# Kernel tuning notes

Measured on AMD Instinct MI355X. Metric: run time of the kernel, lower is better.

Reference implementation:

```python
import jax, jax.numpy as jnp
import numpy as np

GROUP_SIZE = 128


def setup_inputs() -> dict:
    key = jax.random.key(0)
    k1, k2, k3, k4 = jax.random.split(key, 4)
    B, S, IN, OUT = 4, 2048, 4096, 11008
    n_groups = IN // GROUP_SIZE
    x = jax.random.normal(k1, (B, S, IN), dtype=jnp.float32)
    # packed int4: two nibbles per byte -> [OUT, IN//2]
    weight_quantized = jax.random.randint(k2, (OUT, IN // 2), 0, 256, dtype=jnp.int32)
    # per-(row,group) scale > 0 and zero point (stored fp16 in torch, math done in fp32)
    weight_scale = jax.random.uniform(k3, (OUT, n_groups), dtype=jnp.float32, minval=0.001, maxval=0.05)
    weight_zero_point = jax.random.normal(k4, (OUT, n_groups), dtype=jnp.float32) * 0.1
    return {"x": x, "weight_quantized": weight_quantized,
            "weight_scale": weight_scale, "weight_zero_point": weight_zero_point}


def reference(x, weight_quantized, weight_scale, weight_zero_point):
    out_f = weight_quantized.shape[0]
    n_groups = weight_scale.shape[1]
    # unpack nibbles: high first, then low (matches torch.stack([high, low], -1))
    high = (weight_quantized >> 4) & 0xF
    low = weight_quantized & 0xF
    unpacked = jnp.stack([high, low], axis=-1).reshape(out_f, -1).astype(jnp.float32)  # [OUT, IN]
    # grouped dequant: w = q * scale_g + zp_g
    w = unpacked.reshape(out_f, n_groups, GROUP_SIZE)
    w = w * weight_scale[:, :, None] + weight_zero_point[:, :, None]
    w = w.reshape(out_f, -1)  # [OUT, IN]
    # F.linear: x @ w.T
    return jnp.einsum('bsi,oi->bso', x, w)
```

## Files before the change

### kernel.cpp

```cpp
#include <hip/hip_runtime.h>
#include <cstdint>
#include <cstddef>

#define M_TOT 8192
#define N_TOT 11008
#define K_TOT 4096
#define WROW_PACK 2048
#define NG 32

#define BM 256
#define BN 256
#define BKT 32
#define NSLOT 4
#define NT (K_TOT / BKT)
#define NBM2 (M_TOT / BM)
#define NBN2 (N_TOT / BN)
#define NWG2 (NBM2 * NBN2)
#define SLOT_USH 16384
#define LDS_BYTES (NSLOT * SLOT_USH * 2)

typedef __attribute__((ext_vector_type(8))) short short8;
typedef __attribute__((ext_vector_type(4))) float f32x4;
typedef unsigned short ushort_t;

__device__ __forceinline__ unsigned int pack2_bf16(float lo, float hi) {
    return __builtin_amdgcn_perm(__float_as_uint(hi), __float_as_uint(lo), 0x07060302u);
}

__device__ __forceinline__ unsigned int dequant_pair(int q, float s, float z) {
    float wh = (float)(q >> 4) * s + z;
    float wl = (float)(q & 15) * s + z;
    return pack2_bf16(wh, wl);
}

__device__ __forceinline__ void gload_lds16(const void* g, void* l) {
    __builtin_amdgcn_global_load_lds(
        (const __attribute__((address_space(1))) unsigned int*)g,
        (__attribute__((address_space(3))) unsigned int*)l,
        16, 0, 0);
}

__global__ __launch_bounds__(256)
void convert_x_kernel(const float4* __restrict__ xin, uint4* __restrict__ xout) {
    const size_t t = (size_t)blockIdx.x * 256 + threadIdx.x;
    const float4 v0 = xin[2 * t];
    const float4 v1 = xin[2 * t + 1];
    xout[t] = make_uint4(pack2_bf16(v0.x, v0.y), pack2_bf16(v0.z, v0.w),
                         pack2_bf16(v1.x, v1.y), pack2_bf16(v1.z, v1.w));
}

__global__ __launch_bounds__(256)
void dequant_w_kernel(const int4* __restrict__ wq4,
                      const float* __restrict__ wsc,
                      const float* __restrict__ wzp,
                      uint4* __restrict__ wout) {
    const size_t t = (size_t)blockIdx.x * 256 + threadIdx.x;
    const int row = (int)(t >> 9);
    const int c4  = (int)(t & 511);
    const int g   = c4 >> 4;
    const float s = wsc[(size_t)row * NG + g];
    const float z = wzp[(size_t)row * NG + g];
    const int4 q = wq4[t];
    wout[t] = make_uint4(dequant_pair(q.x, s, z), dequant_pair(q.y, s, z),
                         dequant_pair(q.z, s, z), dequant_pair(q.w, s, z));
}

__global__ __launch_bounds__(512, 2)
void gemm_bf16_256(const ushort_t* __restrict__ A,
                   const ushort_t* __restrict__ B,
                   float* __restrict__ out)
{
    extern __shared__ ushort_t lds[];

    const int tid  = threadIdx.x;
    const int lane = tid & 63;
    const int wv   = tid >> 6;
    const int wm   = wv >> 2;
    const int wn   = wv & 3;
    const int l15  = lane & 15;
    const int quad = lane >> 4;

    const int bid = blockIdx.x;
    const int swz = (bid & 7) * (NWG2 >> 3) + (bid >> 3);
    const int bm  = swz / NBN2;
    const int bn  = swz % NBN2;
    const size_t m0 = (size_t)bm * BM;
    const size_t n0 = (size_t)bn * BN;

    const int srow = tid >> 2;
    const int lc   = (tid & 3) ^ (srow & 3);
    const ushort_t* ga0 = A + (m0 + srow) * (size_t)K_TOT + lc * 8;
    const ushort_t* gb0 = B + (n0 + srow) * (size_t)K_TOT + lc * 8;
    const ushort_t* ga1 = ga0 + (size_t)128 * K_TOT;
    const ushort_t* gb1 = gb0 + (size_t)128 * K_TOT;
    const int dst0 = tid * 8;
    const int dst1 = dst0 + 4096;

    const int pco = (quad ^ (l15 & 3)) * 8;
    int aoff[8], boff[4];
#pragma unroll
    for (int mi = 0; mi < 8; ++mi)
        aoff[mi] = (wm * 128 + mi * 16 + l15) * BKT + pco;
#pragma unroll
    for (int ni = 0; ni < 4; ++ni)
        boff[ni] = (wn * 64 + ni * 16 + l15) * BKT + pco;

    f32x4 acc[8][4];
#pragma unroll
    for (int i = 0; i < 8; ++i)
#pragma unroll
        for (int j = 0; j < 4; ++j)
            acc[i][j] = (f32x4)(0.0f);

#pragma unroll
    for (int t = 0; t < 3; ++t) {
        ushort_t* sa = lds + t * SLOT_USH;
        ushort_t* sb = sa + 8192;
        const int ko = t * BKT;
        gload_lds16(ga0 + ko, sa + dst0);
        gload_lds16(ga1 + ko, sa + dst1);
        gload_lds16(gb0 + ko, sb + dst0);
        gload_lds16(gb1 + ko, sb + dst1);
    }
    asm volatile("s_waitcnt vmcnt(8)" ::: "memory");
    __builtin_amdgcn_s_barrier();

#pragma unroll 1
    for (int t = 0; t < NT; ++t) {
        if (t + 3 < NT) {
            const int tp = t + 3;
            ushort_t* sa = lds + (tp & 3) * SLOT_USH;
            ushort_t* sb = sa + 8192;
            const int ko = tp * BKT;
            gload_lds16(ga0 + ko, sa + dst0);
            gload_lds16(ga1 + ko, sa + dst1);
            gload_lds16(gb0 + ko, sb + dst0);
            gload_lds16(gb1 + ko, sb + dst1);
        }

        const ushort_t* sa = lds + (t & 3) * SLOT_USH;
        const ushort_t* sb = sa + 8192;

        short8 af[8], bf[4];
#pragma unroll
        for (int mi = 0; mi < 8; ++mi)
            af[mi] = *reinterpret_cast<const short8*>(sa + aoff[mi]);
#pragma unroll
        for (int ni = 0; ni < 4; ++ni)
            bf[ni] = *reinterpret_cast<const short8*>(sb + boff[ni]);

        __builtin_amdgcn_s_setprio(1);
#pragma unroll
        for (int mi = 0; mi < 8; ++mi)
#pragma unroll
            for (int ni = 0; ni < 4; ++ni)
                acc[mi][ni] = __builtin_amdgcn_mfma_f32_16x16x32_bf16(
                    af[mi], bf[ni], acc[mi][ni], 0, 0, 0);
        __builtin_amdgcn_s_setprio(0);

        if (t + 3 < NT) {
            asm volatile("s_waitcnt vmcnt(8)" ::: "memory");
        } else if (t + 2 < NT) {
            asm volatile("s_waitcnt vmcnt(4)" ::: "memory");
        } else if (t + 1 < NT) {
            asm volatile("s_waitcnt vmcnt(0)" ::: "memory");
        }
        if (t + 1 < NT) __builtin_amdgcn_s_barrier();
    }

#pragma unroll
    for (int mi = 0; mi < 8; ++mi) {
        const size_t row_base = m0 + wm * 128 + mi * 16 + quad * 4;
#pragma unroll
        for (int r = 0; r < 4; ++r) {
            float* dst = out + (row_base + r) * N_TOT + n0 + wn * 64 + l15;
#pragma unroll
            for (int ni = 0; ni < 4; ++ni)
                dst[ni * 16] = acc[mi][ni][r];
        }
    }
}

#define BK 32
#define LDA 40

__global__ __launch_bounds__(256, 2)
void qlinear_kernel(const float* __restrict__ x,
                    const int*   __restrict__ wq,
                    const float* __restrict__ wsc,
                    const float* __restrict__ wzp,
                    float*       __restrict__ out)
{
    __shared__ unsigned short As[128 * LDA];
    __shared__ unsigned short Bs[128 * LDA];

    const int tid  = threadIdx.x;
    const int lane = tid & 63;
    const int wv   = tid >> 6;
    const int wm   = wv >> 1;
    const int wn   = wv & 1;
    const int l15  = lane & 15;
    const int quad = lane >> 4;

    const int n0 = blockIdx.x * 128;
    const int m0 = blockIdx.y * 128;

    const int ar  = tid >> 3;
    const int ac4 = tid & 7;
    const int br  = tid >> 2;
    const int bc  = tid & 3;

    const float4* a_ptrs[4];
#pragma unroll
    for (int i = 0; i < 4; ++i)
        a_ptrs[i] = reinterpret_cast<const float4*>(
                        x + (size_t)(m0 + ar + 32 * i) * K_TOT) + ac4;
    const int4* b_ptrs[2];
#pragma unroll
    for (int i = 0; i < 2; ++i)
        b_ptrs[i] = reinterpret_cast<const int4*>(
                        wq + (size_t)(n0 + br + 64 * i) * WROW_PACK) + bc;

    f32x4 acc[4][4];
#pragma unroll
    for (int i = 0; i < 4; ++i)
#pragma unroll
        for (int j = 0; j < 4; ++j)
            acc[i][j] = (f32x4)(0.0f);

    float s0 = 0.f, z0 = 0.f, s1 = 0.f, z1 = 0.f;

    for (int kt = 0; kt < K_TOT / BK; ++kt) {
        if ((kt & 3) == 0) {
            const int g = kt >> 2;
            s0 = wsc[(size_t)(n0 + br) * NG + g];
            z0 = wzp[(size_t)(n0 + br) * NG + g];
            s1 = wsc[(size_t)(n0 + br + 64) * NG + g];
            z1 = wzp[(size_t)(n0 + br + 64) * NG + g];
        }

#pragma unroll
        for (int i = 0; i < 4; ++i) {
            float4 v = a_ptrs[i][0];
            a_ptrs[i] += 8;
            unsigned int p0 = pack2_bf16(v.x, v.y);
            unsigned int p1 = pack2_bf16(v.z, v.w);
            *reinterpret_cast<uint2*>(&As[(ar + 32 * i) * LDA + ac4 * 4]) =
                make_uint2(p0, p1);
        }

#pragma unroll
        for (int i = 0; i < 2; ++i) {
            int4 q = b_ptrs[i][0];
            b_ptrs[i] += 4;
            const float s = i ? s1 : s0;
            const float z = i ? z1 : z0;
            unsigned int w01 = dequant_pair(q.x, s, z);
            unsigned int w23 = dequant_pair(q.y, s, z);
            unsigned int w45 = dequant_pair(q.z, s, z);
            unsigned int w67 = dequant_pair(q.w, s, z);
            *reinterpret_cast<uint4*>(&Bs[(br + 64 * i) * LDA + bc * 8]) =
                make_uint4(w01, w23, w45, w67);
        }

        __syncthreads();

        short8 af[4], bfr[4];
#pragma unroll
        for (int mi = 0; mi < 4; ++mi)
            af[mi] = *reinterpret_cast<const short8*>(
                &As[(wm * 64 + mi * 16 + l15) * LDA + quad * 8]);
#pragma unroll
        for (int ni = 0; ni < 4; ++ni)
            bfr[ni] = *reinterpret_cast<const short8*>(
                &Bs[(wn * 64 + ni * 16 + l15) * LDA + quad * 8]);
#pragma unroll
        for (int mi = 0; mi < 4; ++mi)
#pragma unroll
            for (int ni = 0; ni < 4; ++ni)
                acc[mi][ni] = __builtin_amdgcn_mfma_f32_16x16x32_bf16(
                    af[mi], bfr[ni], acc[mi][ni], 0, 0, 0);

        __syncthreads();
    }

#pragma unroll
    for (int mi = 0; mi < 4; ++mi) {
        const int row_base = m0 + wm * 64 + mi * 16 + quad * 4;
#pragma unroll
        for (int r = 0; r < 4; ++r) {
            float* dst = out + (size_t)(row_base + r) * N_TOT
                             + n0 + wn * 64 + l15;
#pragma unroll
            for (int ni = 0; ni < 4; ++ni)
                dst[ni * 16] = acc[mi][ni][r];
        }
    }
}

extern "C" void kernel_launch(void* const* d_in, const int* in_sizes, int n_in,
                              void* d_out, int out_size, void* d_ws, size_t ws_size,
                              hipStream_t stream) {
    const float* x   = (const float*)d_in[0];
    const int*   wq  = (const int*)d_in[1];
    const float* wsc = (const float*)d_in[2];
    const float* wzp = (const float*)d_in[3];
    float* out = (float*)d_out;

    const size_t XB = (size_t)M_TOT * K_TOT * 2;
    const size_t WB = (size_t)N_TOT * K_TOT * 2;

    if (ws_size >= XB + WB) {
        static bool attr_set = false;
        if (!attr_set) {
            hipFuncSetAttribute(reinterpret_cast<const void*>(gemm_bf16_256),
                                hipFuncAttributeMaxDynamicSharedMemorySize,
                                LDS_BYTES);
            attr_set = true;
        }
        ushort_t* xb = (ushort_t*)d_ws;
        ushort_t* wb = (ushort_t*)((char*)d_ws + XB);
        convert_x_kernel<<<dim3(M_TOT * K_TOT / (256 * 8)), dim3(256), 0, stream>>>(
            (const float4*)x, (uint4*)xb);
        dequant_w_kernel<<<dim3(N_TOT * WROW_PACK / (256 * 4)), dim3(256), 0, stream>>>(
            (const int4*)wq, wsc, wzp, (uint4*)wb);
        gemm_bf16_256<<<dim3(NWG2), dim3(512), LDS_BYTES, stream>>>(xb, wb, out);
    } else {
        dim3 grid(N_TOT / 128, M_TOT / 128);
        qlinear_kernel<<<grid, dim3(256), 0, stream>>>(x, wq, wsc, wzp, out);
    }
}
```

Baseline: 1.211 ms.

## Split main loop into two MFMA phases and change LDS swizzle pattern

The bf16 GEMM main loop is split into two halves. Each half loads part of the A fragments from LDS, issues half of the next tile's global-to-LDS loads, and runs 16 MFMAs, with extra workgroup barriers between the phases. This interleaves LDS reads, global prefetch issue and MFMA work so waves stay in lockstep and the memory pipes are less bursty. The XOR swizzle used for the LDS writes and fragment reads also changes from row&3 to (row>>1)&3, which is meant to cut LDS bank conflicts. The cost is three extra barriers per iteration.

```diff
diff --git a/kernel.cpp b/kernel.cpp
--- a/kernel.cpp
+++ b/kernel.cpp
@@ -88,7 +88,7 @@
     const size_t n0 = (size_t)bn * BN;
 
     const int srow = tid >> 2;
-    const int lc   = (tid & 3) ^ (srow & 3);
+    const int lc   = (tid & 3) ^ ((tid >> 3) & 3);
     const ushort_t* ga0 = A + (m0 + srow) * (size_t)K_TOT + lc * 8;
     const ushort_t* gb0 = B + (n0 + srow) * (size_t)K_TOT + lc * 8;
     const ushort_t* ga1 = ga0 + (size_t)128 * K_TOT;
@@ -96,7 +96,7 @@
     const int dst0 = tid * 8;
     const int dst1 = dst0 + 4096;
 
-    const int pco = (quad ^ (l15 & 3)) * 8;
+    const int pco = (quad ^ ((l15 >> 1) & 3)) * 8;
     int aoff[8], boff[4];
 #pragma unroll
     for (int mi = 0; mi < 8; ++mi)
@@ -127,37 +127,44 @@
 
 #pragma unroll 1
     for (int t = 0; t < NT; ++t) {
-        if (t + 3 < NT) {
-            const int tp = t + 3;
-            ushort_t* sa = lds + (tp & 3) * SLOT_USH;
-            ushort_t* sb = sa + 8192;
-            const int ko = tp * BKT;
-            gload_lds16(ga0 + ko, sa + dst0);
-            gload_lds16(ga1 + ko, sa + dst1);
-            gload_lds16(gb0 + ko, sb + dst0);
-            gload_lds16(gb1 + ko, sb + dst1);
-        }
-
+        const bool pf = (t + 3 < NT);
+        const int tp = t + 3;
+        ushort_t* pa = lds + (tp & 3) * SLOT_USH;
+        ushort_t* pb = pa + 8192;
+        const int ko = tp * BKT;
         const ushort_t* sa = lds + (t & 3) * SLOT_USH;
         const ushort_t* sb = sa + 8192;
 
-        short8 af[8], bf[4];
-#pragma unroll
-        for (int mi = 0; mi < 8; ++mi)
-            af[mi] = *reinterpret_cast<const short8*>(sa + aoff[mi]);
+        short8 af0[4], bf[4];
+#pragma unroll
+        for (int mi = 0; mi < 4; ++mi)
+            af0[mi] = *reinterpret_cast<const short8*>(sa + aoff[mi]);
 #pragma unroll
         for (int ni = 0; ni < 4; ++ni)
             bf[ni] = *reinterpret_cast<const short8*>(sb + boff[ni]);
-
+        if (pf) {
+            gload_lds16(ga0 + ko, pa + dst0);
+            gload_lds16(ga1 + ko, pa + dst1);
+        }
+        __builtin_amdgcn_s_barrier();
         __builtin_amdgcn_s_setprio(1);
 #pragma unroll
-        for (int mi = 0; mi < 8; ++mi)
+        for (int mi = 0; mi < 4; ++mi)
 #pragma unroll
             for (int ni = 0; ni < 4; ++ni)
                 acc[mi][ni] = __builtin_amdgcn_mfma_f32_16x16x32_bf16(
-                    af[mi], bf[ni], acc[mi][ni], 0, 0, 0);
+                    af0[mi], bf[ni], acc[mi][ni], 0, 0, 0);
         __builtin_amdgcn_s_setprio(0);
-
+        __builtin_amdgcn_s_barrier();
+
+        short8 af1[4];
+#pragma unroll
+        for (int mi = 0; mi < 4; ++mi)
+            af1[mi] = *reinterpret_cast<const short8*>(sa + aoff[4 + mi]);
+        if (pf) {
+            gload_lds16(gb0 + ko, pb + dst0);
+            gload_lds16(gb1 + ko, pb + dst1);
+        }
         if (t + 3 < NT) {
             asm volatile("s_waitcnt vmcnt(8)" ::: "memory");
         } else if (t + 2 < NT) {
@@ -165,6 +172,15 @@
         } else if (t + 1 < NT) {
             asm volatile("s_waitcnt vmcnt(0)" ::: "memory");
         }
+        __builtin_amdgcn_s_barrier();
+        __builtin_amdgcn_s_setprio(1);
+#pragma unroll
+        for (int mi = 0; mi < 4; ++mi)
+#pragma unroll
+            for (int ni = 0; ni < 4; ++ni)
+                acc[4 + mi][ni] = __builtin_amdgcn_mfma_f32_16x16x32_bf16(
+                    af1[mi], bf[ni], acc[4 + mi][ni], 0, 0, 0);
+        __builtin_amdgcn_s_setprio(0);
         if (t + 1 < NT) __builtin_amdgcn_s_barrier();
     }
 
```

After: 1.183 ms. 2.3% less time.
